# Performance work log

Measured on AMD Instinct MI355X. Metric: run time of the kernel, lower is better.

## Reference

```python
import jax, jax.numpy as jnp
import numpy as np

BETA = 0.25


def setup_inputs() -> dict:
    key = jax.random.key(0)
    k1, k2 = jax.random.split(key)
    x = jax.random.normal(k1, (32768, 512), dtype=jnp.float32)
    centroids = jax.random.normal(k2, (8192, 512), dtype=jnp.float32)
    return {"x": x, "centroids": centroids}


def reference(x, centroids):
    # x: [N, D], centroids: [K, D]
    x_norm = jnp.sum(x * x, axis=1, keepdims=True)          # [N, 1]
    c_norm = jnp.sum(centroids * centroids, axis=1)         # [K]
    xy = jnp.einsum('nd,kd->nk', x, centroids)              # [N, K]
    distances = x_norm + c_norm[None, :] - 2.0 * xy         # [N, K]
    indices = jnp.argmin(distances, axis=-1)                # [N]
    q = centroids[indices]                                  # [N, D] gather
    # losses: commitment = mse(sg(q), x); codebook = mse(q, sg(x))
    sg = jax.lax.stop_gradient
    commitment_loss = jnp.mean((sg(q) - x) ** 2)
    codebook_loss = jnp.mean((q - sg(x)) ** 2)
    loss = codebook_loss + BETA * commitment_loss
    # straight-through estimator
    x_q = x + sg(q - x)
    return (x_q, loss, indices)
```

## Files before the change

### kernel.cpp

```cpp
#include <hip/hip_runtime.h>
#include <hip/hip_bf16.h>

#define N_ROWS 32768
#define DIM    512
#define K_CENT 8192

#define LOSS_OFF 16777216u
#define IDX_OFF  16777217u

#define XH_OFF_B   0u
#define CH_OFF_B   33554432u
#define CN_OFF_B   41943040u
#define CAND_OFF_B 41975808u

#define CAND_BYTES 1048576u
#define CN_BYTES   32768u

#define BM 128
#define BN 256
#define KHALF 4096
#define NKT (KHALF / BN)
#define NH  2
#define NSTEP (NKT * 16)

typedef __bf16 bf16x8 __attribute__((ext_vector_type(8)));
typedef float  f32x4  __attribute__((ext_vector_type(4)));

__device__ __forceinline__ unsigned short f2bf(float f) {
    unsigned u = __float_as_uint(f);
    return (unsigned short)((u + 0x7fffu + ((u >> 16) & 1u)) >> 16);
}

__device__ __forceinline__ unsigned umn(unsigned a, unsigned b) { return a < b ? a : b; }
__device__ __forceinline__ unsigned umx(unsigned a, unsigned b) { return a > b ? a : b; }

__device__ __forceinline__ void glds16(void* lds, const void* g) {
    __builtin_amdgcn_global_load_lds(
        (const __attribute__((address_space(1))) unsigned*)g,
        (__attribute__((address_space(3))) unsigned*)lds, 16, 0, 0);
}

__global__ void __launch_bounds__(256) convert_kernel(const float* __restrict__ x,
                                                      const float* __restrict__ c,
                                                      unsigned short* __restrict__ xh,
                                                      unsigned short* __restrict__ ch,
                                                      float* __restrict__ cnp) {
    const int wave = threadIdx.x >> 6, lane = threadIdx.x & 63;
    const int gid = blockIdx.x * 4 + wave;
    if (gid < N_ROWS) {
        const float* p = x + (size_t)gid * DIM + lane * 8;
        float4 a = *(const float4*)p, b = *(const float4*)(p + 4);
        uint4 w;
        w.x = (unsigned)f2bf(a.x) | ((unsigned)f2bf(a.y) << 16);
        w.y = (unsigned)f2bf(a.z) | ((unsigned)f2bf(a.w) << 16);
        w.z = (unsigned)f2bf(b.x) | ((unsigned)f2bf(b.y) << 16);
        w.w = (unsigned)f2bf(b.z) | ((unsigned)f2bf(b.w) << 16);
        *(uint4*)(xh + (size_t)gid * DIM + lane * 8) = w;
    } else {
        const int cr = gid - N_ROWS;
        const float* p = c + (size_t)cr * DIM + lane * 8;
        float4 a = *(const float4*)p, b = *(const float4*)(p + 4);
        uint4 w;
        w.x = (unsigned)f2bf(a.x) | ((unsigned)f2bf(a.y) << 16);
        w.y = (unsigned)f2bf(a.z) | ((unsigned)f2bf(a.w) << 16);
        w.z = (unsigned)f2bf(b.x) | ((unsigned)f2bf(b.y) << 16);
        w.w = (unsigned)f2bf(b.z) | ((unsigned)f2bf(b.w) << 16);
        *(uint4*)(ch + (size_t)cr * DIM + lane * 8) = w;
        float s = a.x*a.x + a.y*a.y + a.z*a.z + a.w*a.w
                + b.x*b.x + b.y*b.y + b.z*b.z + b.w*b.w;
#pragma unroll
        for (int off = 32; off; off >>= 1) s += __shfl_down(s, off, 64);
        if (lane == 0) cnp[cr] = s;
    }
}

__global__ void __launch_bounds__(256, 2) vq_main(const unsigned short* __restrict__ xh,
                                                  const unsigned short* __restrict__ ch,
                                                  const float* __restrict__ cnp,
                                                  float* __restrict__ cand) {
    __shared__ __align__(16) unsigned short xs[3 * 4096];
    __shared__ __align__(16) unsigned short cs[3 * 8192];
    __shared__ unsigned sh_k[2][BM][4];

    const int tid  = threadIdx.x;
    const int wave = tid >> 6, lane = tid & 63;
    const int wm   = wave >> 1, wk = wave & 1;
    const int lr   = lane & 15, quad = lane >> 4;
    const int nbase = blockIdx.x * BM;
    const int h     = blockIdx.y;
    const int kc0   = h * KHALF;

    const int srow16 = lane >> 2;
    const int sswz   = (lane & 3) ^ ((lane >> 3) & 3);
    const unsigned short* xg0 = xh + (size_t)(nbase + wave * 32 + srow16) * DIM + sswz * 8;
    const unsigned short* cg0 = ch + (size_t)(kc0 + wave * 64 + srow16) * DIM + sswz * 8;

    unsigned short* xw = xs + wave * 1024;
    unsigned short* cw = cs + wave * 2048;

#define STAGE(ring, sn_) do {                                                \
        const int ktn_ = (sn_) >> 4;                                         \
        const int dd_  = ((sn_) & 15) * 32;                                  \
        unsigned short* xd_ = xw + (ring) * 4096;                            \
        unsigned short* cd_ = cw + (ring) * 8192;                            \
        const unsigned short* xsrc_ = xg0 + dd_;                             \
        const unsigned short* csrc_ = cg0 + (size_t)ktn_ * (BN * DIM) + dd_; \
        glds16(xd_,        xsrc_);                                           \
        glds16(xd_ + 512,  xsrc_ + 16 * DIM);                                \
        glds16(cd_,        csrc_);                                           \
        glds16(cd_ + 512,  csrc_ + 16 * DIM);                                \
        glds16(cd_ + 1024, csrc_ + 32 * DIM);                                \
        glds16(cd_ + 1536, csrc_ + 48 * DIM);                                \
    } while (0)

    const int sw = (quad ^ ((lr >> 1) & 3)) << 4;
    int aoff[4], boff[8];
#pragma unroll
    for (int mt = 0; mt < 4; ++mt) aoff[mt] = (wm * 64 + mt * 16 + lr) * 64 + sw;
#pragma unroll
    for (int t = 0; t < 8; ++t)    boff[t]  = (wk * 128 + t * 16 + lr) * 64 + sw;

    unsigned k1[4][4], k2[4][4];
#pragma unroll
    for (int mt = 0; mt < 4; ++mt)
#pragma unroll
        for (int r = 0; r < 4; ++r) { k1[mt][r] = 0xFFFFFFFFu; k2[mt][r] = 0xFFFFFFFFu; }

    STAGE(0, 0);
    STAGE(1, 1);
    int rr = 0, rw = 2;

    for (int kt = 0; kt < NKT; ++kt) {
        const int kc = kc0 + kt * BN;
        float cnv[8];
#pragma unroll
        for (int t = 0; t < 8; ++t) cnv[t] = cnp[kc + wk * 128 + t * 16 + lr];

        f32x4 acc[4][8];
#pragma unroll
        for (int mt = 0; mt < 4; ++mt)
#pragma unroll
            for (int t = 0; t < 8; ++t)
                acc[mt][t] = (f32x4){0.f, 0.f, 0.f, 0.f};

#pragma unroll
        for (int j = 0; j < 16; ++j) {
            asm volatile("s_waitcnt vmcnt(6)" ::: "memory");
            __builtin_amdgcn_s_barrier();
            int sn = kt * 16 + j + 2;
            if (sn > NSTEP - 1) sn = NSTEP - 1;
            STAGE(rw, sn);
            const char* xb = (const char*)xs + rr * 8192;
            const char* cb = (const char*)cs + rr * 16384;
            bf16x8 af[4];
#pragma unroll
            for (int mt = 0; mt < 4; ++mt)
                af[mt] = *(const bf16x8*)(xb + aoff[mt]);
#pragma unroll
            for (int t = 0; t < 8; ++t) {
                bf16x8 bf = *(const bf16x8*)(cb + boff[t]);
#pragma unroll
                for (int mt = 0; mt < 4; ++mt)
                    acc[mt][t] = __builtin_amdgcn_mfma_f32_16x16x32_bf16(af[mt], bf, acc[mt][t], 0, 0, 0);
            }
            rr = (rr == 2) ? 0 : rr + 1;
            rw = (rw == 2) ? 0 : rw + 1;
        }

#pragma unroll
        for (int t = 0; t < 8; ++t) {
            const unsigned colb = (unsigned)(kc + wk * 128 + t * 16 + lr);
#pragma unroll
            for (int mt = 0; mt < 4; ++mt)
#pragma unroll
                for (int r = 0; r < 4; ++r) {
                    float d = fmaf(-2.f, acc[mt][t][r], cnv[t]);
                    unsigned u = __float_as_uint(d);
                    u ^= ((unsigned)((int)u >> 31)) | 0x80000000u;
                    unsigned key = (u & 0xFFFFE000u) | colb;
                    unsigned o1 = k1[mt][r];
                    k1[mt][r] = umn(key, o1);
                    k2[mt][r] = umn(umx(key, o1), k2[mt][r]);
                }
        }
    }
#undef STAGE

#pragma unroll
    for (int mt = 0; mt < 4; ++mt)
#pragma unroll
        for (int r = 0; r < 4; ++r) {
            unsigned a0 = k1[mt][r], a1 = k2[mt][r];
            unsigned a2 = 0xFFFFFFFFu, a3 = 0xFFFFFFFFu;
#pragma unroll
            for (int s = 1; s < 16; s <<= 1) {
                unsigned p0 = (unsigned)__shfl_xor((int)a0, s, 64);
                unsigned p1 = (unsigned)__shfl_xor((int)a1, s, 64);
                unsigned p2 = (unsigned)__shfl_xor((int)a2, s, 64);
                unsigned p3 = (unsigned)__shfl_xor((int)a3, s, 64);
                unsigned l0 = umn(a0, p3), l1 = umn(a1, p2);
                unsigned l2 = umn(a2, p1), l3 = umn(a3, p0);
                unsigned c0 = umn(l0, l2), c2 = umx(l0, l2);
                unsigned c1 = umn(l1, l3), c3 = umx(l1, l3);
                a0 = umn(c0, c1); a1 = umx(c0, c1);
                a2 = umn(c2, c3); a3 = umx(c2, c3);
            }
            if (lr == 0) {
                const int rl = wm * 64 + mt * 16 + quad * 4 + r;
                sh_k[wk][rl][0] = a0; sh_k[wk][rl][1] = a1;
                sh_k[wk][rl][2] = a2; sh_k[wk][rl][3] = a3;
            }
        }
    __syncthreads();

    if (tid < BM) {
        unsigned a0 = sh_k[0][tid][0], a1 = sh_k[0][tid][1];
        unsigned a2 = sh_k[0][tid][2], a3 = sh_k[0][tid][3];
        unsigned b0 = sh_k[1][tid][0], b1 = sh_k[1][tid][1];
        unsigned b2 = sh_k[1][tid][2], b3 = sh_k[1][tid][3];
        unsigned l0 = umn(a0, b3), l1 = umn(a1, b2);
        unsigned l2 = umn(a2, b1), l3 = umn(a3, b0);
        unsigned c0 = umn(l0, l2), c2 = umx(l0, l2);
        unsigned c1 = umn(l1, l3), c3 = umx(l1, l3);
        unsigned m0 = umn(c0, c1), m1 = umx(c0, c1);
        unsigned m2 = umn(c2, c3), m3 = umx(c2, c3);
        float4 v;
        v.x = (float)(m0 & 0x1FFFu);
        v.y = (float)(m1 & 0x1FFFu);
        v.z = (float)(m2 & 0x1FFFu);
        v.w = (float)(m3 & 0x1FFFu);
        *(float4*)(cand + (size_t)(nbase + tid) * 8 + h * 4) = v;
    }
}

__global__ void __launch_bounds__(256) vq_refine(const float* __restrict__ x,
                                                 const float* __restrict__ cg,
                                                 const float* __restrict__ cand,
                                                 float* __restrict__ outp,
                                                 int write_xq) {
    __shared__ double ls[4];
    const int wave = threadIdx.x >> 6, lane = threadIdx.x & 63;
    const int n = blockIdx.x * 4 + wave;
    const float* cell = cand + (size_t)n * 8;
    int kid[8];
#pragma unroll
    for (int j = 0; j < 8; ++j) kid[j] = (int)cell[j];

    const float* xr = x + (size_t)n * DIM + lane * 8;
    float4 xa = *(const float4*)xr;
    float4 xb = *(const float4*)(xr + 4);

    float4 ca[8], cb[8];
#pragma unroll
    for (int j = 0; j < 8; ++j) {
        const float* cr = cg + (size_t)kid[j] * DIM + lane * 8;
        ca[j] = *(const float4*)cr;
        cb[j] = *(const float4*)(cr + 4);
    }

    double bd = 1e300; int bi = 0x7fffffff;
    float4 va = xa, vb = xb;
#pragma unroll
    for (int j = 0; j < 8; ++j) {
        const int k = kid[j];
        double s = 0.0, t;
        t = (double)xa.x - (double)ca[j].x; s += t * t;
        t = (double)xa.y - (double)ca[j].y; s += t * t;
        t = (double)xa.z - (double)ca[j].z; s += t * t;
        t = (double)xa.w - (double)ca[j].w; s += t * t;
        t = (double)xb.x - (double)cb[j].x; s += t * t;
        t = (double)xb.y - (double)cb[j].y; s += t * t;
        t = (double)xb.z - (double)cb[j].z; s += t * t;
        t = (double)xb.w - (double)cb[j].w; s += t * t;
#pragma unroll
        for (int off = 32; off; off >>= 1) s += __shfl_down(s, off, 64);
        s = __shfl(s, 0, 64);
        bool w = (s < bd) || (s == bd && k < bi);
        bd = w ? s : bd;
        bi = w ? k : bi;
        va.x = w ? ca[j].x : va.x; va.y = w ? ca[j].y : va.y;
        va.z = w ? ca[j].z : va.z; va.w = w ? ca[j].w : va.w;
        vb.x = w ? cb[j].x : vb.x; vb.y = w ? cb[j].y : vb.y;
        vb.z = w ? cb[j].z : vb.z; vb.w = w ? cb[j].w : vb.w;
    }
    if (write_xq) {
        float* row = outp + (size_t)n * DIM + lane * 8;
        *(float4*)row = va;
        *(float4*)(row + 4) = vb;
    }
    if (lane == 0) { outp[IDX_OFF + n] = (float)bi; ls[wave] = bd; }
    __syncthreads();
    if (threadIdx.x == 0)
        atomicAdd(outp + LOSS_OFF,
                  (float)((ls[0] + ls[1] + ls[2] + ls[3]) * (1.25 / 16777216.0)));
}

__global__ void __launch_bounds__(256) vq_gather(const float* __restrict__ cg,
                                                 float* __restrict__ outp) {
    const int wave = threadIdx.x >> 6, lane = threadIdx.x & 63;
    const int n = blockIdx.x * 4 + wave;
    const int k = (int)outp[IDX_OFF + n];
    const float* cr = cg + (size_t)k * DIM + lane * 8;
    float4 a = *(const float4*)cr;
    float4 b = *(const float4*)(cr + 4);
    float* row = outp + (size_t)n * DIM + lane * 8;
    *(float4*)row = a;
    *(float4*)(row + 4) = b;
}

extern "C" void kernel_launch(void* const* d_in, const int* in_sizes, int n_in,
                              void* d_out, int out_size, void* d_ws, size_t ws_size,
                              hipStream_t stream) {
    const float* x   = (const float*)d_in[0];
    const float* cen = (const float*)d_in[1];
    float* out = (float*)d_out;

    unsigned short* xh  = (unsigned short*)((char*)d_out + XH_OFF_B);
    unsigned short* chp = (unsigned short*)((char*)d_out + CH_OFF_B);

    const int fused = (d_ws != nullptr) && (ws_size >= (size_t)(CAND_BYTES + CN_BYTES));
    float* cand = fused ? (float*)d_ws
                        : (float*)((char*)d_out + CAND_OFF_B);
    float* cnp  = fused ? (float*)((char*)d_ws + CAND_BYTES)
                        : (float*)((char*)d_out + CN_OFF_B);

    hipMemsetAsync((void*)(out + LOSS_OFF), 0, sizeof(float), stream);
    convert_kernel<<<(N_ROWS + K_CENT) / 4, 256, 0, stream>>>(x, cen, xh, chp, cnp);
    dim3 g2(N_ROWS / BM, NH);
    vq_main<<<g2, 256, 0, stream>>>(xh, chp, cnp, cand);
    vq_refine<<<N_ROWS / 4, 256, 0, stream>>>(x, cen, cand, out, fused);
    if (!fused) vq_gather<<<N_ROWS / 4, 256, 0, stream>>>(cen, out);
}
```

Measured before the change: 690.1 us.

## Halve centroid tile width and deepen LDS ring to four stages

```diff
diff --git a/kernel.cpp b/kernel.cpp
--- a/kernel.cpp
+++ b/kernel.cpp
@@ -17,7 +17,7 @@
 #define CN_BYTES   32768u
 
 #define BM 128
-#define BN 256
+#define BN 128
 #define KHALF 4096
 #define NKT (KHALF / BN)
 #define NH  2
@@ -78,8 +78,8 @@
                                                   const unsigned short* __restrict__ ch,
                                                   const float* __restrict__ cnp,
                                                   float* __restrict__ cand) {
-    __shared__ __align__(16) unsigned short xs[3 * 4096];
-    __shared__ __align__(16) unsigned short cs[3 * 8192];
+    __shared__ __align__(16) unsigned short xs[4 * 4096];
+    __shared__ __align__(16) unsigned short cs[4 * 4096];
     __shared__ unsigned sh_k[2][BM][4];
 
     const int tid  = threadIdx.x;
@@ -93,32 +93,29 @@
     const int srow16 = lane >> 2;
     const int sswz   = (lane & 3) ^ ((lane >> 3) & 3);
     const unsigned short* xg0 = xh + (size_t)(nbase + wave * 32 + srow16) * DIM + sswz * 8;
-    const unsigned short* cg0 = ch + (size_t)(kc0 + wave * 64 + srow16) * DIM + sswz * 8;
+    const unsigned short* xg1 = xg0 + (size_t)16 * DIM;
+    const unsigned short* cg0 = ch + (size_t)(kc0 + wave * 32 + srow16) * DIM + sswz * 8;
 
     unsigned short* xw = xs + wave * 1024;
-    unsigned short* cw = cs + wave * 2048;
-
-#define STAGE(ring, sn_) do {                                                \
-        const int ktn_ = (sn_) >> 4;                                         \
-        const int dd_  = ((sn_) & 15) * 32;                                  \
-        unsigned short* xd_ = xw + (ring) * 4096;                            \
-        unsigned short* cd_ = cw + (ring) * 8192;                            \
-        const unsigned short* xsrc_ = xg0 + dd_;                             \
-        const unsigned short* csrc_ = cg0 + (size_t)ktn_ * (BN * DIM) + dd_; \
-        glds16(xd_,        xsrc_);                                           \
-        glds16(xd_ + 512,  xsrc_ + 16 * DIM);                                \
-        glds16(cd_,        csrc_);                                           \
-        glds16(cd_ + 512,  csrc_ + 16 * DIM);                                \
-        glds16(cd_ + 1024, csrc_ + 32 * DIM);                                \
-        glds16(cd_ + 1536, csrc_ + 48 * DIM);                                \
+    unsigned short* cw = cs + wave * 1024;
+
+#define STAGE(ring, ktn, dd) do {                                          \
+        unsigned short* xd_ = xw + (ring) * 4096;                          \
+        unsigned short* cd_ = cw + (ring) * 4096;                          \
+        const unsigned short* cgk_ = cg0 + (size_t)(ktn) * (BN * DIM) + (dd); \
+        glds16(xd_,       xg0 + (dd));                                     \
+        glds16(xd_ + 512, xg1 + (dd));                                     \
+        glds16(cd_,       cgk_);                                           \
+        glds16(cd_ + 512, cgk_ + 16 * DIM);                                \
     } while (0)
 
-    const int sw = (quad ^ ((lr >> 1) & 3)) << 4;
-    int aoff[4], boff[8];
-#pragma unroll
-    for (int mt = 0; mt < 4; ++mt) aoff[mt] = (wm * 64 + mt * 16 + lr) * 64 + sw;
-#pragma unroll
-    for (int t = 0; t < 8; ++t)    boff[t]  = (wk * 128 + t * 16 + lr) * 64 + sw;
+    int aoff[4], boff[4];
+#pragma unroll
+    for (int t = 0; t < 4; ++t) {
+        const int sw = (quad ^ ((lr >> 1) & 3)) << 4;
+        aoff[t] = (wm * 64 + t * 16 + lr) * 64 + sw;
+        boff[t] = (wk * 64 + t * 16 + lr) * 64 + sw;
+    }
 
     unsigned k1[4][4], k2[4][4];
 #pragma unroll
@@ -126,50 +123,54 @@
 #pragma unroll
         for (int r = 0; r < 4; ++r) { k1[mt][r] = 0xFFFFFFFFu; k2[mt][r] = 0xFFFFFFFFu; }
 
-    STAGE(0, 0);
-    STAGE(1, 1);
-    int rr = 0, rw = 2;
+    STAGE(0, 0, 0);
+    STAGE(1, 0, 32);
+    STAGE(2, 0, 64);
+    asm volatile("s_waitcnt vmcnt(0)" ::: "memory");
+    __builtin_amdgcn_s_barrier();
 
     for (int kt = 0; kt < NKT; ++kt) {
         const int kc = kc0 + kt * BN;
-        float cnv[8];
-#pragma unroll
-        for (int t = 0; t < 8; ++t) cnv[t] = cnp[kc + wk * 128 + t * 16 + lr];
-
-        f32x4 acc[4][8];
+        float cnv[4];
+#pragma unroll
+        for (int t = 0; t < 4; ++t) cnv[t] = cnp[kc + wk * 64 + t * 16 + lr];
+
+        f32x4 acc[4][4];
 #pragma unroll
         for (int mt = 0; mt < 4; ++mt)
 #pragma unroll
-            for (int t = 0; t < 8; ++t)
+            for (int t = 0; t < 4; ++t)
                 acc[mt][t] = (f32x4){0.f, 0.f, 0.f, 0.f};
 
-#pragma unroll
+#pragma unroll 4
         for (int j = 0; j < 16; ++j) {
-            asm volatile("s_waitcnt vmcnt(6)" ::: "memory");
+            asm volatile("s_waitcnt vmcnt(8)" ::: "memory");
             __builtin_amdgcn_s_barrier();
-            int sn = kt * 16 + j + 2;
-            if (sn > NSTEP - 1) sn = NSTEP - 1;
-            STAGE(rw, sn);
-            const char* xb = (const char*)xs + rr * 8192;
-            const char* cb = (const char*)cs + rr * 16384;
-            bf16x8 af[4];
-#pragma unroll
-            for (int mt = 0; mt < 4; ++mt)
-                af[mt] = *(const bf16x8*)(xb + aoff[mt]);
-#pragma unroll
-            for (int t = 0; t < 8; ++t) {
-                bf16x8 bf = *(const bf16x8*)(cb + boff[t]);
-#pragma unroll
-                for (int mt = 0; mt < 4; ++mt)
-                    acc[mt][t] = __builtin_amdgcn_mfma_f32_16x16x32_bf16(af[mt], bf, acc[mt][t], 0, 0, 0);
+            {
+                int sn = kt * 16 + j + 3;
+                if (sn > NSTEP - 1) sn = NSTEP - 1;
+                STAGE((kt * 16 + j + 3) & 3, sn >> 4, (sn & 15) * 32);
             }
-            rr = (rr == 2) ? 0 : rr + 1;
-            rw = (rw == 2) ? 0 : rw + 1;
+            const char* xb = (const char*)xs + (j & 3) * 8192;
+            const char* cb = (const char*)cs + (j & 3) * 8192;
+            bf16x8 bfr[4];
+#pragma unroll
+            for (int t = 0; t < 4; ++t)
+                bfr[t] = *(const bf16x8*)(cb + boff[t]);
+            __builtin_amdgcn_s_setprio(1);
+#pragma unroll
+            for (int mt = 0; mt < 4; ++mt) {
+                bf16x8 a = *(const bf16x8*)(xb + aoff[mt]);
+#pragma unroll
+                for (int t = 0; t < 4; ++t)
+                    acc[mt][t] = __builtin_amdgcn_mfma_f32_16x16x32_bf16(a, bfr[t], acc[mt][t], 0, 0, 0);
+            }
+            __builtin_amdgcn_s_setprio(0);
         }
 
 #pragma unroll
-        for (int t = 0; t < 8; ++t) {
-            const unsigned colb = (unsigned)(kc + wk * 128 + t * 16 + lr);
+        for (int t = 0; t < 4; ++t) {
+            const unsigned colb = (unsigned)(kc + wk * 64 + t * 16 + lr);
 #pragma unroll
             for (int mt = 0; mt < 4; ++mt)
 #pragma unroll
```

Result: faster. 614.5 us (-10.9%).
